# Optimization experiments

Hardware: AMD Instinct MI355X
Metric: run time of the kernel (lower is better)

The kernel has to match this reference:

```python
import jax, jax.numpy as jnp
import numpy as np

TEMPERATURE = 0.1
TIME_THRESHOLD = 365
NEG = -1e9  # stands in for -inf; exp(NEG - max) == 0 exactly in fp32
EPS = 1e-12  # F.normalize eps


def setup_inputs() -> dict:
    key = jax.random.key(0)
    k1, k2, k3 = jax.random.split(key, 3)
    B, D = 8192, 128
    embeddings = jax.random.normal(k1, (B, D), dtype=jnp.float32)
    survival_times = jax.random.randint(k2, (B,), 0, 3650, dtype=jnp.int32)
    censor = jax.random.randint(k3, (B,), 0, 2, dtype=jnp.int32)
    return {"embeddings": embeddings, "survival_times": survival_times, "censor": censor}


def reference(embeddings, survival_times, censor):
    B = embeddings.shape[0]
    # L2 normalize rows (torch F.normalize semantics)
    norm = jnp.maximum(jnp.linalg.norm(embeddings, axis=1, keepdims=True), EPS)
    z = embeddings / norm
    # pairwise cosine similarity / temperature: [B, B]
    sim = jnp.einsum('ik,jk->ij', z, z) / TEMPERATURE
    diag = jnp.eye(B, dtype=bool)
    sim = jnp.where(diag, NEG, sim)  # mask self-similarity
    # positive mask: |t_i - t_j| < threshold, i != j, row i uncensored
    tdiff = jnp.abs(survival_times[:, None] - survival_times[None, :])
    pos = (tdiff < TIME_THRESHOLD) & (~diag) & (censor[:, None] == 1)
    # per-row masked logsumexp reductions
    denominator = jax.nn.logsumexp(sim, axis=1)                      # [B]
    numerator = jax.nn.logsumexp(jnp.where(pos, sim, NEG), axis=1)   # [B]
    has_pos = jnp.any(pos, axis=1)
    per_row = jnp.where(has_pos, denominator - numerator, 0.0)
    cnt = jnp.sum(has_pos.astype(jnp.float32))
    return jnp.where(cnt > 0, jnp.sum(per_row) / jnp.maximum(cnt, 1.0), 0.0)
```

## Files before the change

kernel.cpp:

```cpp
#include <hip/hip_runtime.h>
#include <cstdint>

#define BDIM 8192
#define DDIM 128
#define JS 32

#define ZH_OFF 0
#define ZL_OFF (2 * 1024 * 1024)
#define RL_OFF (4 * 1024 * 1024)
#define CNT_OFF (RL_OFF + BDIM * 4)
#define FC_OFF (CNT_OFF + 64)
#define P_OFF (RL_OFF + 65536)
#define PART_OFF (P_OFF + BDIM * JS * 8)

typedef __attribute__((ext_vector_type(8))) short bf16x8;
typedef __attribute__((ext_vector_type(4))) float f32x4;

__device__ __forceinline__ short f2bf(float f) {
  unsigned u = __float_as_uint(f);
  unsigned r = (u + 0x7fffu + ((u >> 16) & 1u)) >> 16;
  return (short)r;
}
__device__ __forceinline__ float bf2f(short h) {
  return __uint_as_float(((unsigned)(unsigned short)h) << 16);
}
__device__ __forceinline__ void gload_lds16(const void* g, void* l) {
  __builtin_amdgcn_global_load_lds(
      (const __attribute__((address_space(1))) unsigned int*)g,
      (__attribute__((address_space(3))) unsigned int*)l, 16, 0, 0);
}


__global__ __launch_bounds__(256) void ck_prep(
    const float* __restrict__ emb, const int* __restrict__ censor,
    short* __restrict__ ZhT, short* __restrict__ ZlT,
    int* __restrict__ rowlist, int* __restrict__ cnt, int* __restrict__ fc)
{
  __shared__ float zl[16][132];
  __shared__ float pr[16][16];
  __shared__ float inv[16];
  __shared__ int wtot[4], woff[4];

  const int t = threadIdx.x;
  if (blockIdx.x == 512) {
    const int lane = t & 63, wv = t >> 6;
    const int4* c4 = (const int4*)(censor + t * 32);
    unsigned fm = 0;
#pragma unroll
    for (int q = 0; q < 8; ++q) {
      const int4 v = c4[q];
      fm |= (unsigned)(v.x == 1) << (q * 4 + 0);
      fm |= (unsigned)(v.y == 1) << (q * 4 + 1);
      fm |= (unsigned)(v.z == 1) << (q * 4 + 2);
      fm |= (unsigned)(v.w == 1) << (q * 4 + 3);
    }
    const int loc = __popc(fm);
    int sc = loc;
#pragma unroll
    for (int m = 1; m < 64; m <<= 1) {
      const int u = __shfl_up(sc, m, 64);
      if (lane >= m) sc += u;
    }
    if (lane == 63) wtot[wv] = sc;
    __syncthreads();
    if (t == 0) {
      int run = 0;
#pragma unroll
      for (int i = 0; i < 4; ++i) { woff[i] = run; run += wtot[i]; }
      fc[0] = 0;
    }
    __syncthreads();
    int off = woff[wv] + sc - loc;
    for (int u = 0; u < 32; ++u)
      if ((fm >> u) & 1) rowlist[off++] = t * 32 + u;
    if (t == 255) cnt[0] = off;
    return;
  }

  const int R = blockIdx.x;
  const int r16 = t >> 4, seg = t & 15;
  const float4* src = (const float4*)(emb + (size_t)(R * 16 + r16) * DDIM + seg * 8);
  const float4 v0 = src[0], v1 = src[1];
  float* zr = &zl[r16][seg * 8];
  zr[0] = v0.x; zr[1] = v0.y; zr[2] = v0.z; zr[3] = v0.w;
  zr[4] = v1.x; zr[5] = v1.y; zr[6] = v1.z; zr[7] = v1.w;
  pr[r16][seg] = v0.x * v0.x + v0.y * v0.y + v0.z * v0.z + v0.w * v0.w +
                 v1.x * v1.x + v1.y * v1.y + v1.z * v1.z + v1.w * v1.w;
  __syncthreads();
  if (t < 16) {
    float ss = 0.f;
#pragma unroll
    for (int s = 0; s < 16; ++s) ss += pr[t][s];
    inv[t] = 1.0f / fmaxf(sqrtf(ss), 1e-12f);
  }
  __syncthreads();
  const int kc = t >> 6, hf = (t >> 4) & 3, rw = t & 15;
  const float iv = inv[rw];
  const float* zs = &zl[rw][(kc * 4 + hf) * 8];
  short hs[8], ls[8];
#pragma unroll
  for (int j = 0; j < 8; ++j) {
    const float z = zs[j] * iv;
    const short h = f2bf(z);
    hs[j] = h;
    ls[j] = f2bf(z - bf2f(h));
  }
  const int dst = R * 2048 + t * 8;
  *(bf16x8*)(ZhT + dst) = *(const bf16x8*)hs;
  *(bf16x8*)(ZlT + dst) = *(const bf16x8*)ls;
}

__global__ __launch_bounds__(256, 2) void ck_main(
    const short* __restrict__ ZhT, const short* __restrict__ ZlT,
    const int* __restrict__ rowlist, const int* __restrict__ cntp,
    const int* __restrict__ times, float2* __restrict__ P2)
{
  __shared__ __align__(16) char lds[65536];
  const int cnt = *cntp;
  const int t = threadIdx.x;
  const int b = blockIdx.x;
  const int it = b >> 5;
  const int js = b & 31;
  if (it * 128 >= cnt) return;
  const int lane = t & 63;
  const int w = t >> 6;
  const int half = lane >> 4;
  const int ll = lane & 15;
  const int jR0 = js * 16;

  int rbase[2];
#pragma unroll
  for (int a = 0; a < 2; ++a) {
    int c = it * 128 + w * 32 + a * 16 + ll;
    if (c >= cnt) c = cnt - 1;
    const int r = rowlist[c];
    rbase[a] = (r >> 4) * 2048 + (r & 15) * 8;
  }
  bf16x8 ah[2][4];
#pragma unroll
  for (int a = 0; a < 2; ++a)
#pragma unroll
    for (int kc = 0; kc < 4; ++kc)
      ah[a][kc] = *(const bf16x8*)(ZhT + rbase[a] + kc * 512 + half * 128);

  int meta[2][4];
#pragma unroll
  for (int a = 0; a < 2; ++a)
#pragma unroll
    for (int r = 0; r < 4; ++r) {
      const int idx = it * 128 + w * 32 + a * 16 + half * 4 + r;
      const bool vi = idx < cnt;
      const int gi = rowlist[vi ? idx : 0];
      const int taP = vi ? (times[gi] + 364) : 50000;
      meta[a][r] = (taP << 16) | (vi ? gi : 0xFFFF);
    }

  float sd[2][4] = {{0.f}}, sn[2][4] = {{0.f}};

  {
    const int c0 = w * 8;
#pragma unroll
    for (int u = 0; u < 8; ++u) {
      const int c = c0 + u, cp = c & 15;
      const short* src = (c < 16) ? ZhT : ZlT;
      const short* gp = src + (size_t)(jR0 + (cp >> 2)) * 2048 + (cp & 3) * 512 + lane * 8;
      gload_lds16(gp, lds + ((c < 16) ? 0 : 16384) + cp * 1024);
    }
  }

  for (int st = 0; st < 4; ++st) {
    __syncthreads();
    if (st < 3) {
      const int pB = ((st + 1) & 1) * 32768;
      const int c0 = w * 8;
#pragma unroll
      for (int u = 0; u < 8; ++u) {
        const int c = c0 + u, cp = c & 15;
        const short* src = (c < 16) ? ZhT : ZlT;
        const short* gp = src + (size_t)(jR0 + (st + 1) * 4 + (cp >> 2)) * 2048 + (cp & 3) * 512 + lane * 8;
        gload_lds16(gp, lds + pB + ((c < 16) ? 0 : 16384) + cp * 1024);
      }
    }

    const char* L = lds + (st & 1) * 32768;
    f32x4 acc[2][4];
#pragma unroll
    for (int a = 0; a < 2; ++a)
#pragma unroll
      for (int bb = 0; bb < 4; ++bb) acc[a][bb] = (f32x4){0.f, 0.f, 0.f, 0.f};

#pragma unroll
    for (int kc = 0; kc < 4; ++kc) {
      bf16x8 alv[2];
#pragma unroll
      for (int a = 0; a < 2; ++a)
        alv[a] = *(const bf16x8*)(ZlT + rbase[a] + kc * 512 + half * 128);
#pragma unroll
      for (int bb = 0; bb < 4; ++bb) {
        const bf16x8 bhv = *(const bf16x8*)(L + bb * 4096 + kc * 1024 + lane * 16);
        const bf16x8 blv = *(const bf16x8*)(L + 16384 + bb * 4096 + kc * 1024 + lane * 16);
        acc[0][bb] = __builtin_amdgcn_mfma_f32_16x16x32_bf16(ah[0][kc], bhv, acc[0][bb], 0, 0, 0);
        acc[1][bb] = __builtin_amdgcn_mfma_f32_16x16x32_bf16(ah[1][kc], bhv, acc[1][bb], 0, 0, 0);
        acc[0][bb] = __builtin_amdgcn_mfma_f32_16x16x32_bf16(ah[0][kc], blv, acc[0][bb], 0, 0, 0);
        acc[1][bb] = __builtin_amdgcn_mfma_f32_16x16x32_bf16(ah[1][kc], blv, acc[1][bb], 0, 0, 0);
        acc[0][bb] = __builtin_amdgcn_mfma_f32_16x16x32_bf16(alv[0], bhv, acc[0][bb], 0, 0, 0);
        acc[1][bb] = __builtin_amdgcn_mfma_f32_16x16x32_bf16(alv[1], bhv, acc[1][bb], 0, 0, 0);
      }
    }

    const int jb = js * 256 + st * 64;
    int tJ[4];
#pragma unroll
    for (int bb = 0; bb < 4; ++bb) tJ[bb] = times[jb + bb * 16 + ll];
#pragma unroll
    for (int a = 0; a < 2; ++a)
#pragma unroll
      for (int r = 0; r < 4; ++r) {
        const int m_ = meta[a][r];
        const int gi = m_ & 0xFFFF;
        const unsigned taP = ((unsigned)m_) >> 16;
        float d = 0.f, n = 0.f;
#pragma unroll
        for (int bb = 0; bb < 4; ++bb) {
          const int jgb = jb + bb * 16 + ll;
          float pv = __expf(fmaf(acc[a][bb][r], 10.f, -10.f));
          pv = (gi == jgb) ? 0.f : pv;
          d += pv;
          n += ((unsigned)(taP - (unsigned)tJ[bb]) <= 728u) ? pv : 0.f;
        }
        sd[a][r] += d;
        sn[a][r] += n;
      }
  }

#pragma unroll
  for (int a = 0; a < 2; ++a)
#pragma unroll
    for (int r = 0; r < 4; ++r) {
      float d = sd[a][r], n = sn[a][r];
#pragma unroll
      for (int m = 1; m <= 8; m <<= 1) {
        d += __shfl_xor(d, m, 64);
        n += __shfl_xor(n, m, 64);
      }
      const int idx = it * 128 + w * 32 + a * 16 + half * 4 + r;
      if (ll == 0 && idx < cnt) P2[(size_t)idx * JS + js] = make_float2(d, n);
    }
}

__global__ __launch_bounds__(256) void ck_fin(
    const float2* __restrict__ P2, const int* __restrict__ cntp,
    float2* __restrict__ part, int* __restrict__ fc, float* __restrict__ out)
{
  const int cnt = *cntp;
  const int t = threadIdx.x;
  const int idx = blockIdx.x * 256 + t;
  float lsum = 0.f, lcnt = 0.f;
  if (idx < cnt) {
    const float4* p = (const float4*)(P2 + (size_t)idx * JS);
    float d = 0.f, n = 0.f;
#pragma unroll
    for (int u = 0; u < 16; ++u) {
      const float4 v = p[u];
      d += v.x + v.z;
      n += v.y + v.w;
    }
    if (n > 0.f) { lsum = logf(d) - logf(n); lcnt = 1.f; }
  }
  __shared__ float s1[256], s2[256];
  __shared__ int amLast;
  s1[t] = lsum; s2[t] = lcnt;
  __syncthreads();
  for (int s = 128; s > 0; s >>= 1) {
    if (t < s) { s1[t] += s1[t + s]; s2[t] += s2[t + s]; }
    __syncthreads();
  }
  if (t == 0) {
    part[blockIdx.x] = make_float2(s1[0], s2[0]);
    __threadfence();
    amLast = (atomicAdd(fc, 1) == gridDim.x - 1);
  }
  __syncthreads();
  if (amLast) {
    __threadfence();
    float s = 0.f, c = 0.f;
    if (t < 32) { const float2 v = part[t]; s = v.x; c = v.y; }
    if (t < 64) {
#pragma unroll
      for (int m = 1; m < 64; m <<= 1) {
        s += __shfl_xor(s, m, 64);
        c += __shfl_xor(c, m, 64);
      }
      if (t == 0) out[0] = (c > 0.f) ? s / fmaxf(c, 1.f) : 0.f;
    }
  }
}

extern "C" void kernel_launch(void* const* d_in, const int* in_sizes, int n_in,
                              void* d_out, int out_size, void* d_ws, size_t ws_size,
                              hipStream_t stream) {
  const float* emb  = (const float*)d_in[0];
  const int* times  = (const int*)d_in[1];
  const int* censor = (const int*)d_in[2];
  float* out = (float*)d_out;

  char* ws = (char*)d_ws;
  short* ZhT    = (short*)(ws + ZH_OFF);
  short* ZlT    = (short*)(ws + ZL_OFF);
  int* rowlist  = (int*)(ws + RL_OFF);
  int* cntp     = (int*)(ws + CNT_OFF);
  int* fc       = (int*)(ws + FC_OFF);
  float2* P2    = (float2*)(ws + P_OFF);
  float2* part  = (float2*)(ws + PART_OFF);

  ck_prep<<<513, 256, 0, stream>>>(emb, censor, ZhT, ZlT, rowlist, cntp, fc);
  ck_main<<<64 * 32, 256, 0, stream>>>(ZhT, ZlT, rowlist, cntp, times, P2);
  ck_fin<<<32, 256, 0, stream>>>(P2, cntp, part, fc, out);
}
```

Before: 111.0 us.

## Use symmetric two-term bf16 split to cut MFMAs and fuse finalize into main

Replaces the hi/lo bf16 split with a hi/mid encoding (m = bf16(2z - h)) so the similarity is computed with two MFMA products instead of three, halving the exp scale accordingly. The separate finalize kernel is folded into the main kernel via a last-block atomic counter, and per-stage times loads are hoisted. This reduces matrix-core work and one kernel launch, at the cost of some precision in the dot products and a serial single-block tail reduction.

```diff
diff --git a/kernel.cpp b/kernel.cpp
--- a/kernel.cpp
+++ b/kernel.cpp
@@ -6,12 +6,11 @@
 #define JS 32
 
 #define ZH_OFF 0
-#define ZL_OFF (2 * 1024 * 1024)
+#define ZM_OFF (2 * 1024 * 1024)
 #define RL_OFF (4 * 1024 * 1024)
 #define CNT_OFF (RL_OFF + BDIM * 4)
 #define FC_OFF (CNT_OFF + 64)
 #define P_OFF (RL_OFF + 65536)
-#define PART_OFF (P_OFF + BDIM * JS * 8)
 
 typedef __attribute__((ext_vector_type(8))) short bf16x8;
 typedef __attribute__((ext_vector_type(4))) float f32x4;
@@ -33,7 +32,7 @@
 
 __global__ __launch_bounds__(256) void ck_prep(
     const float* __restrict__ emb, const int* __restrict__ censor,
-    short* __restrict__ ZhT, short* __restrict__ ZlT,
+    short* __restrict__ ZhT, short* __restrict__ ZmT,
     int* __restrict__ rowlist, int* __restrict__ cnt, int* __restrict__ fc)
 {
   __shared__ float zl[16][132];
@@ -97,23 +96,24 @@
   const int kc = t >> 6, hf = (t >> 4) & 3, rw = t & 15;
   const float iv = inv[rw];
   const float* zs = &zl[rw][(kc * 4 + hf) * 8];
-  short hs[8], ls[8];
+  short hs[8], ms[8];
 #pragma unroll
   for (int j = 0; j < 8; ++j) {
     const float z = zs[j] * iv;
     const short h = f2bf(z);
     hs[j] = h;
-    ls[j] = f2bf(z - bf2f(h));
+    ms[j] = f2bf(2.f * z - bf2f(h));
   }
   const int dst = R * 2048 + t * 8;
   *(bf16x8*)(ZhT + dst) = *(const bf16x8*)hs;
-  *(bf16x8*)(ZlT + dst) = *(const bf16x8*)ls;
+  *(bf16x8*)(ZmT + dst) = *(const bf16x8*)ms;
 }
 
 __global__ __launch_bounds__(256, 2) void ck_main(
-    const short* __restrict__ ZhT, const short* __restrict__ ZlT,
+    const short* __restrict__ ZhT, const short* __restrict__ ZmT,
     const int* __restrict__ rowlist, const int* __restrict__ cntp,
-    const int* __restrict__ times, float2* __restrict__ P2)
+    const int* __restrict__ times, float2* __restrict__ P2,
+    int* __restrict__ fc, float* __restrict__ out)
 {
   __shared__ __align__(16) char lds[65536];
   const int cnt = *cntp;
@@ -121,178 +121,161 @@
   const int b = blockIdx.x;
   const int it = b >> 5;
   const int js = b & 31;
-  if (it * 128 >= cnt) return;
   const int lane = t & 63;
   const int w = t >> 6;
   const int half = lane >> 4;
   const int ll = lane & 15;
   const int jR0 = js * 16;
 
-  int rbase[2];
-#pragma unroll
-  for (int a = 0; a < 2; ++a) {
-    int c = it * 128 + w * 32 + a * 16 + ll;
-    if (c >= cnt) c = cnt - 1;
-    const int r = rowlist[c];
-    rbase[a] = (r >> 4) * 2048 + (r & 15) * 8;
-  }
-  bf16x8 ah[2][4];
-#pragma unroll
-  for (int a = 0; a < 2; ++a)
-#pragma unroll
-    for (int kc = 0; kc < 4; ++kc)
-      ah[a][kc] = *(const bf16x8*)(ZhT + rbase[a] + kc * 512 + half * 128);
-
-  int meta[2][4];
-#pragma unroll
-  for (int a = 0; a < 2; ++a)
-#pragma unroll
-    for (int r = 0; r < 4; ++r) {
-      const int idx = it * 128 + w * 32 + a * 16 + half * 4 + r;
-      const bool vi = idx < cnt;
-      const int gi = rowlist[vi ? idx : 0];
-      const int taP = vi ? (times[gi] + 364) : 50000;
-      meta[a][r] = (taP << 16) | (vi ? gi : 0xFFFF);
-    }
-
-  float sd[2][4] = {{0.f}}, sn[2][4] = {{0.f}};
-
-  {
-    const int c0 = w * 8;
-#pragma unroll
-    for (int u = 0; u < 8; ++u) {
-      const int c = c0 + u, cp = c & 15;
-      const short* src = (c < 16) ? ZhT : ZlT;
-      const short* gp = src + (size_t)(jR0 + (cp >> 2)) * 2048 + (cp & 3) * 512 + lane * 8;
-      gload_lds16(gp, lds + ((c < 16) ? 0 : 16384) + cp * 1024);
-    }
-  }
-
-  for (int st = 0; st < 4; ++st) {
-    __syncthreads();
-    if (st < 3) {
-      const int pB = ((st + 1) & 1) * 32768;
+  if (it * 128 < cnt) {
+    int rbase[2];
+#pragma unroll
+    for (int a = 0; a < 2; ++a) {
+      int c = it * 128 + w * 32 + a * 16 + ll;
+      if (c >= cnt) c = cnt - 1;
+      const int r = rowlist[c];
+      rbase[a] = (r >> 4) * 2048 + (r & 15) * 8;
+    }
+    bf16x8 ah[2][4], am[2][4];
+#pragma unroll
+    for (int a = 0; a < 2; ++a)
+#pragma unroll
+      for (int kc = 0; kc < 4; ++kc) {
+        ah[a][kc] = *(const bf16x8*)(ZhT + rbase[a] + kc * 512 + half * 128);
+        am[a][kc] = *(const bf16x8*)(ZmT + rbase[a] + kc * 512 + half * 128);
+      }
+
+    int meta[2][4];
+#pragma unroll
+    for (int a = 0; a < 2; ++a)
+#pragma unroll
+      for (int r = 0; r < 4; ++r) {
+        const int idx = it * 128 + w * 32 + a * 16 + half * 4 + r;
+        const bool vi = idx < cnt;
+        const int gi = rowlist[vi ? idx : 0];
+        const int taP = vi ? (times[gi] + 364) : 50000;
+        meta[a][r] = (taP << 16) | (vi ? gi : 0xFFFF);
+      }
+
+    int tJ[4][4];
+#pragma unroll
+    for (int st = 0; st < 4; ++st)
+#pragma unroll
+      for (int bb = 0; bb < 4; ++bb)
+        tJ[st][bb] = times[js * 256 + st * 64 + bb * 16 + ll];
+
+    float sd[2][4] = {{0.f}}, sn[2][4] = {{0.f}};
+
+    {
       const int c0 = w * 8;
 #pragma unroll
       for (int u = 0; u < 8; ++u) {
         const int c = c0 + u, cp = c & 15;
-        const short* src = (c < 16) ? ZhT : ZlT;
-        const short* gp = src + (size_t)(jR0 + (st + 1) * 4 + (cp >> 2)) * 2048 + (cp & 3) * 512 + lane * 8;
-        gload_lds16(gp, lds + pB + ((c < 16) ? 0 : 16384) + cp * 1024);
-      }
-    }
-
-    const char* L = lds + (st & 1) * 32768;
-    f32x4 acc[2][4];
+        const short* src = (c < 16) ? ZhT : ZmT;
+        const short* gp = src + (size_t)(jR0 + (cp >> 2)) * 2048 + (cp & 3) * 512 + lane * 8;
+        gload_lds16(gp, lds + ((c < 16) ? 0 : 16384) + cp * 1024);
+      }
+    }
+
+    for (int st = 0; st < 4; ++st) {
+      __syncthreads();
+      if (st < 3) {
+        const int pB = ((st + 1) & 1) * 32768;
+        const int c0 = w * 8;
+#pragma unroll
+        for (int u = 0; u < 8; ++u) {
+          const int c = c0 + u, cp = c & 15;
+          const short* src = (c < 16) ? ZhT : ZmT;
+          const short* gp = src + (size_t)(jR0 + (st + 1) * 4 + (cp >> 2)) * 2048 + (cp & 3) * 512 + lane * 8;
+          gload_lds16(gp, lds + pB + ((c < 16) ? 0 : 16384) + cp * 1024);
+        }
+      }
+
+      const char* L = lds + (st & 1) * 32768;
+      f32x4 acc[2][4];
+#pragma unroll
+      for (int a = 0; a < 2; ++a)
+#pragma unroll
+        for (int bb = 0; bb < 4; ++bb) acc[a][bb] = (f32x4){0.f, 0.f, 0.f, 0.f};
+
+#pragma unroll
+      for (int kc = 0; kc < 4; ++kc) {
+#pragma unroll
+        for (int bb = 0; bb < 4; ++bb) {
+          const bf16x8 bhv = *(const bf16x8*)(L + bb * 4096 + kc * 1024 + lane * 16);
+          const bf16x8 bmv = *(const bf16x8*)(L + 16384 + bb * 4096 + kc * 1024 + lane * 16);
+          acc[0][bb] = __builtin_amdgcn_mfma_f32_16x16x32_bf16(ah[0][kc], bmv, acc[0][bb], 0, 0, 0);
+          acc[1][bb] = __builtin_amdgcn_mfma_f32_16x16x32_bf16(ah[1][kc], bmv, acc[1][bb], 0, 0, 0);
+          acc[0][bb] = __builtin_amdgcn_mfma_f32_16x16x32_bf16(am[0][kc], bhv, acc[0][bb], 0, 0, 0);
+          acc[1][bb] = __builtin_amdgcn_mfma_f32_16x16x32_bf16(am[1][kc], bhv, acc[1][bb], 0, 0, 0);
+        }
+      }
+
+      const int jb = js * 256 + st * 64;
+#pragma unroll
+      for (int a = 0; a < 2; ++a)
+#pragma unroll
+        for (int r = 0; r < 4; ++r) {
+          const int m_ = meta[a][r];
+          const int gi = m_ & 0xFFFF;
+          const unsigned taP = ((unsigned)m_) >> 16;
+          float d = 0.f, n = 0.f;
+#pragma unroll
+          for (int bb = 0; bb < 4; ++bb) {
+            const int jgb = jb + bb * 16 + ll;
+            float pv = __expf(fmaf(acc[a][bb][r], 5.f, -10.f));
+            pv = (gi == jgb) ? 0.f : pv;
+            d += pv;
+            n += ((unsigned)(taP - (unsigned)tJ[st][bb]) <= 728u) ? pv : 0.f;
+          }
+          sd[a][r] += d;
+          sn[a][r] += n;
+        }
+    }
+
 #pragma unroll
     for (int a = 0; a < 2; ++a)
 #pragma unroll
-      for (int bb = 0; bb < 4; ++bb) acc[a][bb] = (f32x4){0.f, 0.f, 0.f, 0.f};
-
-#pragma unroll
-    for (int kc = 0; kc < 4; ++kc) {
-      bf16x8 alv[2];
-#pragma unroll
-      for (int a = 0; a < 2; ++a)
-        alv[a] = *(const bf16x8*)(ZlT + rbase[a] + kc * 512 + half * 128);
-#pragma unroll
-      for (int bb = 0; bb < 4; ++bb) {
-        const bf16x8 bhv = *(const bf16x8*)(L + bb * 4096 + kc * 1024 + lane * 16);
-        const bf16x8 blv = *(const bf16x8*)(L + 16384 + bb * 4096 + kc * 1024 + lane * 16);
-        acc[0][bb] = __builtin_amdgcn_mfma_f32_16x16x32_bf16(ah[0][kc], bhv, acc[0][bb], 0, 0, 0);
-        acc[1][bb] = __builtin_amdgcn_mfma_f32_16x16x32_bf16(ah[1][kc], bhv, acc[1][bb], 0, 0, 0);
-        acc[0][bb] = __builtin_amdgcn_mfma_f32_16x16x32_bf16(ah[0][kc], blv, acc[0][bb], 0, 0, 0);
-        acc[1][bb] = __builtin_amdgcn_mfma_f32_16x16x32_bf16(ah[1][kc], blv, acc[1][bb], 0, 0, 0);
-        acc[0][bb] = __builtin_amdgcn_mfma_f32_16x16x32_bf16(alv[0], bhv, acc[0][bb], 0, 0, 0);
-        acc[1][bb] = __builtin_amdgcn_mfma_f32_16x16x32_bf16(alv[1], bhv, acc[1][bb], 0, 0, 0);
-      }
-    }
-
-    const int jb = js * 256 + st * 64;
-    int tJ[4];
-#pragma unroll
-    for (int bb = 0; bb < 4; ++bb) tJ[bb] = times[jb + bb * 16 + ll];
-#pragma unroll
-    for (int a = 0; a < 2; ++a)
-#pragma unroll
       for (int r = 0; r < 4; ++r) {
-        const int m_ = meta[a][r];
-        const int gi = m_ & 0xFFFF;
-        const unsigned taP = ((unsigned)m_) >> 16;
-        float d = 0.f, n = 0.f;
-#pragma unroll
-        for (int bb = 0; bb < 4; ++bb) {
-          const int jgb = jb + bb * 16 + ll;
-          float pv = __expf(fmaf(acc[a][bb][r], 10.f, -10.f));
-          pv = (gi == jgb) ? 0.f : pv;
-          d += pv;
-          n += ((unsigned)(taP - (unsigned)tJ[bb]) <= 728u) ? pv : 0.f;
+        float d = sd[a][r], n = sn[a][r];
+#pragma unroll
+        for (int m = 1; m <= 8; m <<= 1) {
+          d += __shfl_xor(d, m, 64);
+          n += __shfl_xor(n, m, 64);
         }
-        sd[a][r] += d;
-        sn[a][r] += n;
-      }
-  }
-
-#pragma unroll
-  for (int a = 0; a < 2; ++a)
-#pragma unroll
-    for (int r = 0; r < 4; ++r) {
-      float d = sd[a][r], n = sn[a][r];
-#pragma unroll
-      for (int m = 1; m <= 8; m <<= 1) {
-        d += __shfl_xor(d, m, 64);
-        n += __shfl_xor(n, m, 64);
-      }
-      const int idx = it * 128 + w * 32 + a * 16 + half * 4 + r;
-      if (ll == 0 && idx < cnt) P2[(size_t)idx * JS + js] = make_float2(d, n);
-    }
-}
-
-__global__ __launch_bounds__(256) void ck_fin(
-    const float2* __restrict__ P2, const int* __restrict__ cntp,
-    float2* __restrict__ part, int* __restrict__ fc, float* __restrict__ out)
-{
-  const int cnt = *cntp;
-  const int t = threadIdx.x;
-  const int idx = blockIdx.x * 256 + t;
-  float lsum = 0.f, lcnt = 0.f;
-  if (idx < cnt) {
-    const float4* p = (const float4*)(P2 + (size_t)idx * JS);
-    float d = 0.f, n = 0.f;
-#pragma unroll
-    for (int u = 0; u < 16; ++u) {
-      const float4 v = p[u];
-      d += v.x + v.z;
-      n += v.y + v.w;
-    }
-    if (n > 0.f) { lsum = logf(d) - logf(n); lcnt = 1.f; }
-  }
-  __shared__ float s1[256], s2[256];
-  __shared__ int amLast;
-  s1[t] = lsum; s2[t] = lcnt;
+        const int idx = it * 128 + w * 32 + a * 16 + half * 4 + r;
+        if (ll == 0 && idx < cnt) P2[(size_t)idx * JS + js] = make_float2(d, n);
+      }
+  }
+
+  __threadfence();
   __syncthreads();
-  for (int s = 128; s > 0; s >>= 1) {
-    if (t < s) { s1[t] += s1[t + s]; s2[t] += s2[t + s]; }
+  int* flag = (int*)(lds + 2048);
+  if (t == 0) *flag = (atomicAdd(fc, 1) == (int)gridDim.x - 1);
+  __syncthreads();
+  if (*flag) {
+    __threadfence();
+    float lsum = 0.f, lcnt = 0.f;
+    for (int idx = t; idx < cnt; idx += 256) {
+      const float4* p = (const float4*)(P2 + (size_t)idx * JS);
+      float d = 0.f, n = 0.f;
+#pragma unroll
+      for (int u = 0; u < 16; ++u) {
+        const float4 v = p[u];
+        d += v.x + v.z;
+        n += v.y + v.w;
+      }
+      if (n > 0.f) { lsum += logf(d) - logf(n); lcnt += 1.f; }
+    }
+    float* s1 = (float*)lds;
+    float* s2 = (float*)(lds + 1024);
+    s1[t] = lsum; s2[t] = lcnt;
     __syncthreads();
-  }
-  if (t == 0) {
-    part[blockIdx.x] = make_float2(s1[0], s2[0]);
-    __threadfence();
-    amLast = (atomicAdd(fc, 1) == gridDim.x - 1);
-  }
-  __syncthreads();
-  if (amLast) {
-    __threadfence();
-    float s = 0.f, c = 0.f;
-    if (t < 32) { const float2 v = part[t]; s = v.x; c = v.y; }
-    if (t < 64) {
-#pragma unroll
-      for (int m = 1; m < 64; m <<= 1) {
-        s += __shfl_xor(s, m, 64);
-        c += __shfl_xor(c, m, 64);
-      }
-      if (t == 0) out[0] = (c > 0.f) ? s / fmaxf(c, 1.f) : 0.f;
-    }
+    for (int s = 128; s > 0; s >>= 1) {
+      if (t < s) { s1[t] += s1[t + s]; s2[t] += s2[t + s]; }
+      __syncthreads();
+    }
+    if (t == 0) out[0] = (s2[0] > 0.f) ? s1[0] / fmaxf(s2[0], 1.f) : 0.f;
   }
 }
 
@@ -306,14 +289,12 @@
 
   char* ws = (char*)d_ws;
   short* ZhT    = (short*)(ws + ZH_OFF);
-  short* ZlT    = (short*)(ws + ZL_OFF);
+  short* ZmT    = (short*)(ws + ZM_OFF);
   int* rowlist  = (int*)(ws + RL_OFF);
   int* cntp     = (int*)(ws + CNT_OFF);
   int* fc       = (int*)(ws + FC_OFF);
   float2* P2    = (float2*)(ws + P_OFF);
-  float2* part  = (float2*)(ws + PART_OFF);
-
-  ck_prep<<<513, 256, 0, stream>>>(emb, censor, ZhT, ZlT, rowlist, cntp, fc);
-  ck_main<<<64 * 32, 256, 0, stream>>>(ZhT, ZlT, rowlist, cntp, times, P2);
-  ck_fin<<<32, 256, 0, stream>>>(P2, cntp, part, fc, out);
-}
+
+  ck_prep<<<513, 256, 0, stream>>>(emb, censor, ZhT, ZmT, rowlist, cntp, fc);
+  ck_main<<<64 * 32, 256, 0, stream>>>(ZhT, ZmT, rowlist, cntp, times, P2, fc, out);
+}
```

New measurement: 278.0 us. +150.4%, slower.
